# Kernel optimization log

Hardware: AMD Instinct MI355X
Metric: run time of the kernel (lower is better)

The kernel has to match this reference:

```python
import jax, jax.numpy as jnp
import numpy as np

N = 8192
E = 131072
IN = 512
H = 8
C = 128
HC = H * C
EPS = 1e-5
NEG_SLOPE = 0.2


def _gatv2(x, src, dst, Wl, bl, Wr, br, att, bias):
    """GATv2Conv (PyG semantics, concat=True, self-loops already in src/dst)."""
    n = x.shape[0]
    xl = (x @ Wl + bl).reshape(n, H, C)  # source transform (lin_l)
    xr = (x @ Wr + br).reshape(n, H, C)  # dest transform (lin_r)
    m = xl[src] + xr[dst]                # [E,H,C] per-edge message
    e = jnp.einsum('ehc,hc->eh', jax.nn.leaky_relu(m, NEG_SLOPE), att)  # [E,H]
    # segment softmax over destination nodes
    emax = jax.ops.segment_max(e, dst, num_segments=n)
    w = jnp.exp(e - emax[dst])
    denom = jax.ops.segment_sum(w, dst, num_segments=n)
    alpha = w / denom[dst]               # [E,H]
    out = jax.ops.segment_sum(alpha[:, :, None] * xl[src], dst, num_segments=n)
    return out.reshape(n, HC) + bias


def _bn(x, gamma, beta):
    mu = jnp.mean(x, axis=0)
    var = jnp.mean((x - mu) ** 2, axis=0)
    return (x - mu) * jax.lax.rsqrt(var + EPS) * gamma + beta


def setup_inputs() -> dict:
    key = jax.random.key(0)
    ks = jax.random.split(key, 16)
    s = 0.05
    return {
        'x': jax.random.normal(ks[0], (N, IN), jnp.float32),
        'edge_index': jax.random.randint(ks[1], (2, E), 0, N, jnp.int32),
        'W1l': jax.random.normal(ks[2], (IN, HC), jnp.float32) * s,
        'b1l': jnp.zeros((HC,), jnp.float32),
        'W1r': jax.random.normal(ks[3], (IN, HC), jnp.float32) * s,
        'b1r': jnp.zeros((HC,), jnp.float32),
        'att1': jax.random.normal(ks[4], (H, C), jnp.float32) * s,
        'bias1': jnp.zeros((HC,), jnp.float32),
        'g1': jnp.ones((HC,), jnp.float32),
        'beta1': jnp.zeros((HC,), jnp.float32),
        'W2l': jax.random.normal(ks[5], (HC, HC), jnp.float32) * s,
        'b2l': jnp.zeros((HC,), jnp.float32),
        'W2r': jax.random.normal(ks[6], (HC, HC), jnp.float32) * s,
        'b2r': jnp.zeros((HC,), jnp.float32),
        'att2': jax.random.normal(ks[7], (H, C), jnp.float32) * s,
        'bias2': jnp.zeros((HC,), jnp.float32),
        'g2': jnp.ones((HC,), jnp.float32),
        'beta2': jnp.zeros((HC,), jnp.float32),
    }


def reference(x, edge_index, W1l, b1l, W1r, b1r, att1, bias1, g1, beta1,
              W2l, b2l, W2r, b2r, att2, bias2, g2, beta2):
    n = x.shape[0]
    loops = jnp.arange(n, dtype=edge_index.dtype)
    src = jnp.concatenate([edge_index[0], loops])
    dst = jnp.concatenate([edge_index[1], loops])
    h = _gatv2(x, src, dst, W1l, b1l, W1r, b1r, att1, bias1)
    h = jax.nn.elu(_bn(h, g1, beta1))
    h = _gatv2(h, src, dst, W2l, b2l, W2r, b2r, att2, bias2)
    h = jax.nn.elu(_bn(h, g2, beta2))
    return h
```

## Files before the change

kernel.cpp:

```cpp
#include <hip/hip_runtime.h>
#include <stdint.h>

#define NN     8192
#define NEDGE  131072
#define NETOT  (NEDGE + NN)
#define K_IN   512
#define HC_    1024
#define NOUT   2048
#define BNEPS  1e-5f
#define SLOPE  0.2f

typedef __bf16 bf16x8 __attribute__((ext_vector_type(8)));
typedef float  f32x4  __attribute__((ext_vector_type(4)));
typedef float  f32x2  __attribute__((ext_vector_type(2)));

__device__ __forceinline__ float bf2f(unsigned short u) {
  union { uint32_t u; float f; } c; c.u = ((uint32_t)u) << 16; return c.f;
}
__device__ __forceinline__ unsigned short f2bf(float f) {
  union { float f; uint32_t u; } c; c.f = f;
  uint32_t r = c.u + 0x7fffu + ((c.u >> 16) & 1u);
  return (unsigned short)(r >> 16);
}
__device__ __forceinline__ f32x2 upk2(uint32_t u) {
  union { uint32_t u; float f; } a, b;
  a.u = u << 16; b.u = u & 0xffff0000u;
  f32x2 r; r.x = a.f; r.y = b.f; return r;
}

__device__ __forceinline__ void gload16(const void* g, void* l) {
  __builtin_amdgcn_global_load_lds(
      (const __attribute__((address_space(1))) uint32_t*)g,
      (__attribute__((address_space(3))) uint32_t*)l, 16, 0, 0);
}

#define SBAR() do { asm volatile("" ::: "memory"); __builtin_amdgcn_s_barrier(); asm volatile("" ::: "memory"); } while (0)

__global__ __launch_bounds__(256) void k_cvt_bf16(const float* __restrict__ in,
                                                  unsigned short* __restrict__ out, int n4) {
  int i = blockIdx.x * 256 + threadIdx.x;
  if (i >= n4) return;
  float4 v = *(const float4*)&in[(size_t)i * 4];
  ushort4 o;
  o.x = f2bf(v.x); o.y = f2bf(v.y); o.z = f2bf(v.z); o.w = f2bf(v.w);
  *(ushort4*)&out[(size_t)i * 4] = o;
}

__global__ __launch_bounds__(256) void k_transpose_bf16(const float* __restrict__ W,
                                                        unsigned short* __restrict__ Wt,
                                                        int K, int N) {
  __shared__ float tile[32][33];
  int n0 = blockIdx.x * 32, k0 = blockIdx.y * 32;
  int tx = threadIdx.x & 31, ty = threadIdx.x >> 5;
  for (int i = ty; i < 32; i += 8)
    tile[i][tx] = W[(size_t)(k0 + i) * N + n0 + tx];
  __syncthreads();
  for (int i = ty; i < 32; i += 8)
    Wt[(size_t)(n0 + i) * K + k0 + tx] = f2bf(tile[tx][i]);
}

__global__ __launch_bounds__(256) void k_hist(const int* __restrict__ ei, int* __restrict__ cnt) {
  int i = blockIdx.x * 256 + threadIdx.x;
  if (i >= NETOT) return;
  int d = (i < NEDGE) ? ei[NEDGE + i] : (i - NEDGE);
  atomicAdd(&cnt[d], 1);
}

__global__ __launch_bounds__(256) void k_scan(const int* __restrict__ cnt,
                                              int* __restrict__ rowptr,
                                              int* __restrict__ cursor) {
  __shared__ int part[256];
  int t = threadIdx.x;
  int base = t * 32;
  int s = 0;
  for (int i = 0; i < 32; ++i) s += cnt[base + i];
  part[t] = s;
  __syncthreads();
  for (int off = 1; off < 256; off <<= 1) {
    int u = (t >= off) ? part[t - off] : 0;
    __syncthreads();
    part[t] += u;
    __syncthreads();
  }
  int run = part[t] - s;
  for (int i = 0; i < 32; ++i) {
    rowptr[base + i] = run;
    cursor[base + i] = run;
    run += cnt[base + i];
  }
  if (t == 255) rowptr[NN] = run;
}

__global__ __launch_bounds__(256) void k_scatter(const int* __restrict__ ei,
                                                 int* __restrict__ cursor,
                                                 int* __restrict__ srcs) {
  int i = blockIdx.x * 256 + threadIdx.x;
  if (i >= NETOT) return;
  int s, d;
  if (i < NEDGE) { s = ei[i]; d = ei[NEDGE + i]; }
  else           { s = d = i - NEDGE; }
  int pos = atomicAdd(&cursor[d], 1);
  srcs[pos] = s;
}

__global__ __launch_bounds__(512, 2) void k_gemm256(const unsigned short* __restrict__ A,
                                                    const unsigned short* __restrict__ Bt,
                                                    const float* __restrict__ biasL,
                                                    const float* __restrict__ biasR,
                                                    unsigned short* __restrict__ C,
                                                    int K) {
  __shared__ unsigned short lA[2][256 * 64];
  __shared__ unsigned short lB[2][256 * 64];

  const int bid = blockIdx.x;
  const int xcd = bid & 7, idx = bid >> 3;
  const int m0 = (xcd * 4 + (idx & 3)) * 256;
  const int n0 = (idx >> 2) * 256;

  const int tid = threadIdx.x;
  const int l   = tid & 63;
  const int wv  = tid >> 6;
  const int wm  = wv >> 2, wn = wv & 3;
  const int l15 = l & 15, l4 = l >> 4;

  const int srow = tid >> 3;
  const int ssgk = (tid & 7) ^ (srow & 7);

  const f32x4 vzero = {0.f, 0.f, 0.f, 0.f};
  f32x4 acc[8][4];
#pragma unroll
  for (int i = 0; i < 8; ++i)
#pragma unroll
    for (int j = 0; j < 4; ++j) acc[i][j] = vzero;

  bf16x8 a2[8];
  bf16x8 bb[2][4];

  auto stageA = [&](int kt, int h) {
    const int buf = kt & 1;
    const size_t go = (size_t)(m0 + h * 128 + srow) * K + (size_t)kt * 64 + ssgk * 8;
    unsigned short* lp = &lA[buf][h * 8192 + tid * 8];
    gload16(&A[go], lp);
    gload16(&A[go + (size_t)64 * K], lp + 4096);
  };
  auto stageB = [&](int kt, int h) {
    const int buf = kt & 1;
    const size_t go = (size_t)(n0 + h * 128 + srow) * K + (size_t)kt * 64 + ssgk * 8;
    unsigned short* lp = &lB[buf][h * 8192 + tid * 8];
    gload16(&Bt[go], lp);
    gload16(&Bt[go + (size_t)64 * K], lp + 4096);
  };
  auto readA = [&](int buf, int qm) {
#pragma unroll
    for (int fm = 0; fm < 4; ++fm)
#pragma unroll
      for (int kk = 0; kk < 2; ++kk) {
        int r = wm * 128 + (qm * 4 + fm) * 16 + l15;
        int g = (kk * 4 + l4) ^ (r & 7);
        a2[fm * 2 + kk] = *(const bf16x8*)&lA[buf][r * 64 + g * 8];
      }
  };
  auto readB = [&](int buf, int qn) {
#pragma unroll
    for (int fn = 0; fn < 2; ++fn)
#pragma unroll
      for (int kk = 0; kk < 2; ++kk) {
        int r = wn * 64 + (qn * 2 + fn) * 16 + l15;
        int g = (kk * 4 + l4) ^ (r & 7);
        bb[qn][fn * 2 + kk] = *(const bf16x8*)&lB[buf][r * 64 + g * 8];
      }
  };
  auto quad = [&](int qm, int qn) {
    __builtin_amdgcn_s_setprio(1);
#pragma unroll
    for (int fm = 0; fm < 4; ++fm)
#pragma unroll
      for (int fn = 0; fn < 2; ++fn)
#pragma unroll
        for (int kk = 0; kk < 2; ++kk)
          acc[qm * 4 + fm][qn * 2 + fn] = __builtin_amdgcn_mfma_f32_16x16x32_bf16(
              a2[fm * 2 + kk], bb[qn][fn * 2 + kk], acc[qm * 4 + fm][qn * 2 + fn], 0, 0, 0);
    __builtin_amdgcn_s_setprio(0);
  };

  const int NT = K >> 6;

  stageA(0, 0); stageA(0, 1); stageB(0, 0); stageB(0, 1);
  if (NT > 1) stageA(1, 0);
  asm volatile("s_waitcnt vmcnt(2)" ::: "memory");
  SBAR();

  for (int t = 0; t < NT; ++t) {
    const int buf = t & 1;
    readA(buf, 0); readB(buf, 0);
    if (t + 1 < NT) stageA(t + 1, 1);
    SBAR();
    quad(0, 0);
    SBAR();
    readB(buf, 1);
    if (t + 1 < NT) stageB(t + 1, 0);
    SBAR();
    quad(0, 1);
    SBAR();
    readA(buf, 1);
    if (t + 1 < NT) stageB(t + 1, 1);
    SBAR();
    quad(1, 0);
    SBAR();
    if (t + 2 < NT) stageA(t + 2, 0);
    asm volatile("s_waitcnt vmcnt(2)" ::: "memory");
    SBAR();
    quad(1, 1);
    SBAR();
  }

  const float* bias = (n0 < HC_) ? biasL : (biasR - HC_);
#pragma unroll
  for (int fm = 0; fm < 8; ++fm) {
#pragma unroll
    for (int fn = 0; fn < 4; ++fn) {
      int col = n0 + wn * 64 + fn * 16 + l15;
      float bv = bias[col];
#pragma unroll
      for (int j = 0; j < 4; ++j) {
        int row = m0 + wm * 128 + fm * 16 + l4 * 4 + j;
        C[(size_t)row * NOUT + col] = f2bf(acc[fm][fn][j] + bv);
      }
    }
  }
}

__global__ __launch_bounds__(256) void k_edge_agg(const unsigned short* __restrict__ XLR,
                                                  const float* __restrict__ att,
                                                  const float* __restrict__ bias,
                                                  const int* __restrict__ rowptr,
                                                  const int* __restrict__ srcs,
                                                  float* __restrict__ out) {
  const int d   = blockIdx.x;
  const int tid = threadIdx.x;
  const int g   = tid >> 6;
  const int l   = tid & 63;
  const int c0  = l * 16;

  f32x2 attv[8], xrv[8];
  {
    const f32x2* ap = (const f32x2*)&att[c0];
#pragma unroll
    for (int q = 0; q < 8; ++q) attv[q] = ap[q];
    const uint4* rp = (const uint4*)&XLR[(size_t)d * NOUT + HC_ + c0];
    uint4 u0 = rp[0], u1 = rp[1];
    xrv[0] = upk2(u0.x); xrv[1] = upk2(u0.y); xrv[2] = upk2(u0.z); xrv[3] = upk2(u0.w);
    xrv[4] = upk2(u1.x); xrv[5] = upk2(u1.y); xrv[6] = upk2(u1.z); xrv[7] = upk2(u1.w);
  }

  f32x2 acc2[8];
#pragma unroll
  for (int j = 0; j < 8; ++j) acc2[j] = (f32x2){0.f, 0.f};
  float den = 0.f;

  const int beg = rowptr[d], end = rowptr[d + 1];
  int i = beg + g;
  uint4 u0n, u1n;
  if (i < end) {
    const uint4* rp = (const uint4*)&XLR[(size_t)srcs[i] * NOUT + c0];
    u0n = rp[0]; u1n = rp[1];
  }
  while (i < end) {
    uint4 u0 = u0n, u1 = u1n;
    int nx = i + 4;
    if (nx < end) {
      const uint4* rp = (const uint4*)&XLR[(size_t)srcs[nx] * NOUT + c0];
      u0n = rp[0]; u1n = rp[1];
    }
    f32x2 x[8];
    x[0] = upk2(u0.x); x[1] = upk2(u0.y); x[2] = upk2(u0.z); x[3] = upk2(u0.w);
    x[4] = upk2(u1.x); x[5] = upk2(u1.y); x[6] = upk2(u1.z); x[7] = upk2(u1.w);
    f32x2 ps = (f32x2){0.f, 0.f};
#pragma unroll
    for (int j = 0; j < 8; ++j) {
      f32x2 m  = x[j] + xrv[j];
      f32x2 lr = __builtin_elementwise_max(m, m * SLOPE);
      ps = lr * attv[j] + ps;
    }
    float p = ps.x + ps.y;
    p += __shfl_xor(p, 1);
    p += __shfl_xor(p, 2);
    p += __shfl_xor(p, 4);
    float wgt = __expf(p);
    den += wgt;
    f32x2 w2 = (f32x2){wgt, wgt};
#pragma unroll
    for (int j = 0; j < 8; ++j) acc2[j] = w2 * x[j] + acc2[j];
    i = nx;
  }

  __shared__ float sacc[4][64][17];
  __shared__ float sden[4][64];
#pragma unroll
  for (int j = 0; j < 8; ++j) {
    sacc[g][l][j * 2]     = acc2[j].x;
    sacc[g][l][j * 2 + 1] = acc2[j].y;
  }
  sden[g][l] = den;
  __syncthreads();

  const int c  = tid * 4;
  const int hl = (c >> 7) * 8;
  float dtot = sden[0][hl] + sden[1][hl] + sden[2][hl] + sden[3][hl];
  float inv  = 1.0f / dtot;
  float4 bv  = *(const float4*)&bias[c];
  float o[4];
#pragma unroll
  for (int j = 0; j < 4; ++j) {
    int cc = c + j, ll = cc >> 4, jj = cc & 15;
    float s = sacc[0][ll][jj] + sacc[1][ll][jj] + sacc[2][ll][jj] + sacc[3][ll][jj];
    o[j] = s * inv;
  }
  float4 ov = {o[0] + bv.x, o[1] + bv.y, o[2] + bv.z, o[3] + bv.w};
  *(float4*)&out[(size_t)d * HC_ + c] = ov;
}

__global__ __launch_bounds__(256) void k_colstats(const float* __restrict__ X,
                                                  float* __restrict__ stats) {
  int col = blockIdx.x * 256 + threadIdx.x;
  int r0 = blockIdx.y * 128;
  float s = 0.f, q = 0.f;
  for (int r = r0; r < r0 + 128; ++r) {
    float v = X[(size_t)r * HC_ + col];
    s += v;
    q += v * v;
  }
  atomicAdd(&stats[col], s);
  atomicAdd(&stats[HC_ + col], q);
}

template <bool OUT_BF16>
__global__ __launch_bounds__(256) void k_bn_elu(const float* __restrict__ X,
                                                const float* __restrict__ stats,
                                                const float* __restrict__ gamma,
                                                const float* __restrict__ beta,
                                                void* __restrict__ outp) {
  size_t idx = (size_t)blockIdx.x * 256 + threadIdx.x;
  size_t e0 = idx * 4;
  int col = (int)(e0 & (HC_ - 1));
  float4 xv = *(const float4*)&X[e0];
  float xs[4] = {xv.x, xv.y, xv.z, xv.w};
  float os[4];
  const float rn = 1.0f / (float)NN;
#pragma unroll
  for (int j = 0; j < 4; ++j) {
    int c = col + j;
    float mu = stats[c] * rn;
    float var = stats[HC_ + c] * rn - mu * mu;
    float v = (xs[j] - mu) * rsqrtf(var + BNEPS) * gamma[c] + beta[c];
    os[j] = v > 0.f ? v : (__expf(v) - 1.f);
  }
  if (OUT_BF16) {
    ushort4 o;
    o.x = f2bf(os[0]); o.y = f2bf(os[1]); o.z = f2bf(os[2]); o.w = f2bf(os[3]);
    *(ushort4*)&((unsigned short*)outp)[e0] = o;
  } else {
    float4 o = {os[0], os[1], os[2], os[3]};
    *(float4*)&((float*)outp)[e0] = o;
  }
}

extern "C" void kernel_launch(void* const* d_in, const int* in_sizes, int n_in,
                              void* d_out, int out_size, void* d_ws, size_t ws_size,
                              hipStream_t stream) {
  const float* x     = (const float*)d_in[0];
  const int*   ei    = (const int*)d_in[1];
  const float* W1l   = (const float*)d_in[2];
  const float* b1l   = (const float*)d_in[3];
  const float* W1r   = (const float*)d_in[4];
  const float* b1r   = (const float*)d_in[5];
  const float* att1  = (const float*)d_in[6];
  const float* bias1 = (const float*)d_in[7];
  const float* g1    = (const float*)d_in[8];
  const float* be1   = (const float*)d_in[9];
  const float* W2l   = (const float*)d_in[10];
  const float* b2l   = (const float*)d_in[11];
  const float* W2r   = (const float*)d_in[12];
  const float* b2r   = (const float*)d_in[13];
  const float* att2  = (const float*)d_in[14];
  const float* bias2 = (const float*)d_in[15];
  const float* g2    = (const float*)d_in[16];
  const float* be2   = (const float*)d_in[17];
  float* out = (float*)d_out;

  char* wsb = (char*)d_ws;
  size_t o = 0;
  auto alloc = [&](size_t b) {
    void* p = wsb + o;
    o = (o + b + 255) & ~(size_t)255;
    return p;
  };
  unsigned short* xbf  = (unsigned short*)alloc((size_t)NN * K_IN * 2);
  unsigned short* wT1  = (unsigned short*)alloc((size_t)NOUT * K_IN * 2);
  unsigned short* wT2  = (unsigned short*)alloc((size_t)NOUT * HC_ * 2);
  unsigned short* XLR  = (unsigned short*)alloc((size_t)NN * NOUT * 2);
  unsigned short* h1bf = (unsigned short*)alloc((size_t)NN * HC_ * 2);
  int* cnt     = (int*)alloc((size_t)NN * 4);
  int* rowptr  = (int*)alloc((size_t)(NN + 1) * 4);
  int* cursor  = (int*)alloc((size_t)NN * 4);
  int* srcs    = (int*)alloc((size_t)NETOT * 4);
  float* stats = (float*)alloc((size_t)2 * HC_ * 4);

  hipMemsetAsync(cnt, 0, (size_t)NN * 4, stream);
  hipMemsetAsync(stats, 0, (size_t)2 * HC_ * 4, stream);

  k_cvt_bf16<<<(NN * K_IN / 4 + 255) / 256, 256, 0, stream>>>(x, xbf, NN * K_IN / 4);
  k_transpose_bf16<<<dim3(HC_ / 32, K_IN / 32), 256, 0, stream>>>(W1l, wT1, K_IN, HC_);
  k_transpose_bf16<<<dim3(HC_ / 32, K_IN / 32), 256, 0, stream>>>(W1r, wT1 + (size_t)HC_ * K_IN, K_IN, HC_);
  k_transpose_bf16<<<dim3(HC_ / 32, HC_ / 32), 256, 0, stream>>>(W2l, wT2, HC_, HC_);
  k_transpose_bf16<<<dim3(HC_ / 32, HC_ / 32), 256, 0, stream>>>(W2r, wT2 + (size_t)HC_ * HC_, HC_, HC_);

  k_hist<<<(NETOT + 255) / 256, 256, 0, stream>>>(ei, cnt);
  k_scan<<<1, 256, 0, stream>>>(cnt, rowptr, cursor);
  k_scatter<<<(NETOT + 255) / 256, 256, 0, stream>>>(ei, cursor, srcs);

  k_gemm256<<<256, 512, 0, stream>>>(xbf, wT1, b1l, b1r, XLR, K_IN);
  k_edge_agg<<<NN, 256, 0, stream>>>(XLR, att1, bias1, rowptr, srcs, out);
  k_colstats<<<dim3(HC_ / 256, NN / 128), 256, 0, stream>>>(out, stats);
  k_bn_elu<true><<<NN * HC_ / 4 / 256, 256, 0, stream>>>(out, stats, g1, be1, h1bf);

  k_gemm256<<<256, 512, 0, stream>>>(h1bf, wT2, b2l, b2r, XLR, HC_);
  k_edge_agg<<<NN, 256, 0, stream>>>(XLR, att2, bias2, rowptr, srcs, out);
  hipMemsetAsync(stats, 0, (size_t)2 * HC_ * 4, stream);
  k_colstats<<<dim3(HC_ / 256, NN / 128), 256, 0, stream>>>(out, stats);
  k_bn_elu<false><<<NN * HC_ / 4 / 256, 256, 0, stream>>>(out, stats, g2, be2, out);
}
```

Before: 252.1 us.

## Assign one wavefront per destination node and store layer-1 activations in bf16

The edge aggregation kernel now gives each wavefront a whole destination node and processes four nodes per block. This removes the shared-memory cross-wave reduction and the block barrier, and it prefetches two source rows ahead. Layer-1 aggregation output is written as bf16 and reused in place for colstats and BN/ELU, which cuts the fp32 intermediate traffic. Weight transposes are merged into two launches via a z grid dimension. The trade-offs are less memory-level parallelism per node for high-degree nodes and extra bf16 rounding before batch-norm statistics.

```diff
diff --git a/kernel.cpp b/kernel.cpp
--- a/kernel.cpp
+++ b/kernel.cpp
@@ -12,7 +12,6 @@
 
 typedef __bf16 bf16x8 __attribute__((ext_vector_type(8)));
 typedef float  f32x4  __attribute__((ext_vector_type(4)));
-typedef float  f32x2  __attribute__((ext_vector_type(2)));
 
 __device__ __forceinline__ float bf2f(unsigned short u) {
   union { uint32_t u; float f; } c; c.u = ((uint32_t)u) << 16; return c.f;
@@ -22,10 +21,10 @@
   uint32_t r = c.u + 0x7fffu + ((c.u >> 16) & 1u);
   return (unsigned short)(r >> 16);
 }
-__device__ __forceinline__ f32x2 upk2(uint32_t u) {
+__device__ __forceinline__ void unpack2(uint32_t u, float& lo, float& hi) {
   union { uint32_t u; float f; } a, b;
   a.u = u << 16; b.u = u & 0xffff0000u;
-  f32x2 r; r.x = a.f; r.y = b.f; return r;
+  lo = a.f; hi = b.f;
 }
 
 __device__ __forceinline__ void gload16(const void* g, void* l) {
@@ -46,17 +45,20 @@
   *(ushort4*)&out[(size_t)i * 4] = o;
 }
 
-__global__ __launch_bounds__(256) void k_transpose_bf16(const float* __restrict__ W,
-                                                        unsigned short* __restrict__ Wt,
-                                                        int K, int N) {
+__global__ __launch_bounds__(256) void k_transpose2_bf16(const float* __restrict__ Wa,
+                                                         const float* __restrict__ Wb,
+                                                         unsigned short* __restrict__ Wt,
+                                                         int K, int N) {
   __shared__ float tile[32][33];
+  const float* W = blockIdx.z ? Wb : Wa;
+  unsigned short* dst = Wt + (size_t)blockIdx.z * N * K;
   int n0 = blockIdx.x * 32, k0 = blockIdx.y * 32;
   int tx = threadIdx.x & 31, ty = threadIdx.x >> 5;
   for (int i = ty; i < 32; i += 8)
     tile[i][tx] = W[(size_t)(k0 + i) * N + n0 + tx];
   __syncthreads();
   for (int i = ty; i < 32; i += 8)
-    Wt[(size_t)(n0 + i) * K + k0 + tx] = f2bf(tile[tx][i]);
+    dst[(size_t)(n0 + i) * K + k0 + tx] = f2bf(tile[tx][i]);
 }
 
 __global__ __launch_bounds__(256) void k_hist(const int* __restrict__ ei, int* __restrict__ cnt) {
@@ -230,103 +232,118 @@
   }
 }
 
+template <bool OUT_BF16>
 __global__ __launch_bounds__(256) void k_edge_agg(const unsigned short* __restrict__ XLR,
                                                   const float* __restrict__ att,
                                                   const float* __restrict__ bias,
                                                   const int* __restrict__ rowptr,
                                                   const int* __restrict__ srcs,
-                                                  float* __restrict__ out) {
-  const int d   = blockIdx.x;
+                                                  void* __restrict__ outp) {
   const int tid = threadIdx.x;
-  const int g   = tid >> 6;
+  const int d   = blockIdx.x * 4 + (tid >> 6);
   const int l   = tid & 63;
   const int c0  = l * 16;
 
-  f32x2 attv[8], xrv[8];
+  float attv[16], xrv[16];
   {
-    const f32x2* ap = (const f32x2*)&att[c0];
-#pragma unroll
-    for (int q = 0; q < 8; ++q) attv[q] = ap[q];
+    const float4* ap = (const float4*)&att[c0];
+#pragma unroll
+    for (int q = 0; q < 4; ++q) {
+      float4 v = ap[q];
+      attv[q * 4 + 0] = v.x; attv[q * 4 + 1] = v.y;
+      attv[q * 4 + 2] = v.z; attv[q * 4 + 3] = v.w;
+    }
     const uint4* rp = (const uint4*)&XLR[(size_t)d * NOUT + HC_ + c0];
     uint4 u0 = rp[0], u1 = rp[1];
-    xrv[0] = upk2(u0.x); xrv[1] = upk2(u0.y); xrv[2] = upk2(u0.z); xrv[3] = upk2(u0.w);
-    xrv[4] = upk2(u1.x); xrv[5] = upk2(u1.y); xrv[6] = upk2(u1.z); xrv[7] = upk2(u1.w);
-  }
-
-  f32x2 acc2[8];
-#pragma unroll
-  for (int j = 0; j < 8; ++j) acc2[j] = (f32x2){0.f, 0.f};
+    unpack2(u0.x, xrv[0], xrv[1]);   unpack2(u0.y, xrv[2], xrv[3]);
+    unpack2(u0.z, xrv[4], xrv[5]);   unpack2(u0.w, xrv[6], xrv[7]);
+    unpack2(u1.x, xrv[8], xrv[9]);   unpack2(u1.y, xrv[10], xrv[11]);
+    unpack2(u1.z, xrv[12], xrv[13]); unpack2(u1.w, xrv[14], xrv[15]);
+  }
+
+  float acc[16];
+#pragma unroll
+  for (int j = 0; j < 16; ++j) acc[j] = 0.f;
   float den = 0.f;
 
   const int beg = rowptr[d], end = rowptr[d + 1];
-  int i = beg + g;
-  uint4 u0n, u1n;
-  if (i < end) {
-    const uint4* rp = (const uint4*)&XLR[(size_t)srcs[i] * NOUT + c0];
-    u0n = rp[0]; u1n = rp[1];
-  }
-  while (i < end) {
-    uint4 u0 = u0n, u1 = u1n;
-    int nx = i + 4;
-    if (nx < end) {
-      const uint4* rp = (const uint4*)&XLR[(size_t)srcs[nx] * NOUT + c0];
-      u0n = rp[0]; u1n = rp[1];
-    }
-    f32x2 x[8];
-    x[0] = upk2(u0.x); x[1] = upk2(u0.y); x[2] = upk2(u0.z); x[3] = upk2(u0.w);
-    x[4] = upk2(u1.x); x[5] = upk2(u1.y); x[6] = upk2(u1.z); x[7] = upk2(u1.w);
-    f32x2 ps = (f32x2){0.f, 0.f};
-#pragma unroll
-    for (int j = 0; j < 8; ++j) {
-      f32x2 m  = x[j] + xrv[j];
-      f32x2 lr = __builtin_elementwise_max(m, m * SLOPE);
-      ps = lr * attv[j] + ps;
-    }
-    float p = ps.x + ps.y;
+  uint4 b0u0, b0u1, b1u0, b1u1;
+  {
+    const uint4* rp = (const uint4*)&XLR[(size_t)srcs[beg] * NOUT + c0];
+    b0u0 = rp[0]; b0u1 = rp[1];
+  }
+  if (beg + 1 < end) {
+    const uint4* rp = (const uint4*)&XLR[(size_t)srcs[beg + 1] * NOUT + c0];
+    b1u0 = rp[0]; b1u1 = rp[1];
+  }
+  int s2 = (beg + 2 < end) ? srcs[beg + 2] : 0;
+
+  for (int i = beg; i < end; ++i) {
+    uint4 u0 = b0u0, u1 = b0u1;
+    b0u0 = b1u0; b0u1 = b1u1;
+    if (i + 2 < end) {
+      const uint4* rp = (const uint4*)&XLR[(size_t)s2 * NOUT + c0];
+      b1u0 = rp[0]; b1u1 = rp[1];
+    }
+    s2 = (i + 3 < end) ? srcs[i + 3] : 0;
+
+    float x[16];
+    unpack2(u0.x, x[0], x[1]);   unpack2(u0.y, x[2], x[3]);
+    unpack2(u0.z, x[4], x[5]);   unpack2(u0.w, x[6], x[7]);
+    unpack2(u1.x, x[8], x[9]);   unpack2(u1.y, x[10], x[11]);
+    unpack2(u1.z, x[12], x[13]); unpack2(u1.w, x[14], x[15]);
+    float p = 0.f;
+#pragma unroll
+    for (int j = 0; j < 16; ++j) {
+      float m  = x[j] + xrv[j];
+      float lr = fmaxf(m, SLOPE * m);
+      p = fmaf(lr, attv[j], p);
+    }
     p += __shfl_xor(p, 1);
     p += __shfl_xor(p, 2);
     p += __shfl_xor(p, 4);
     float wgt = __expf(p);
     den += wgt;
-    f32x2 w2 = (f32x2){wgt, wgt};
-#pragma unroll
-    for (int j = 0; j < 8; ++j) acc2[j] = w2 * x[j] + acc2[j];
-    i = nx;
-  }
-
-  __shared__ float sacc[4][64][17];
-  __shared__ float sden[4][64];
-#pragma unroll
-  for (int j = 0; j < 8; ++j) {
-    sacc[g][l][j * 2]     = acc2[j].x;
-    sacc[g][l][j * 2 + 1] = acc2[j].y;
-  }
-  sden[g][l] = den;
-  __syncthreads();
-
-  const int c  = tid * 4;
-  const int hl = (c >> 7) * 8;
-  float dtot = sden[0][hl] + sden[1][hl] + sden[2][hl] + sden[3][hl];
-  float inv  = 1.0f / dtot;
-  float4 bv  = *(const float4*)&bias[c];
-  float o[4];
-#pragma unroll
-  for (int j = 0; j < 4; ++j) {
-    int cc = c + j, ll = cc >> 4, jj = cc & 15;
-    float s = sacc[0][ll][jj] + sacc[1][ll][jj] + sacc[2][ll][jj] + sacc[3][ll][jj];
-    o[j] = s * inv;
-  }
-  float4 ov = {o[0] + bv.x, o[1] + bv.y, o[2] + bv.z, o[3] + bv.w};
-  *(float4*)&out[(size_t)d * HC_ + c] = ov;
-}
-
-__global__ __launch_bounds__(256) void k_colstats(const float* __restrict__ X,
+#pragma unroll
+    for (int j = 0; j < 16; ++j) acc[j] = fmaf(wgt, x[j], acc[j]);
+  }
+
+  float inv = 1.0f / den;
+  if (OUT_BF16) {
+    unsigned short* op = (unsigned short*)outp + (size_t)d * HC_ + c0;
+#pragma unroll
+    for (int q = 0; q < 2; ++q) {
+      ushort4 o0, o1;
+      const float4 bv0 = ((const float4*)&bias[c0])[q * 2];
+      const float4 bv1 = ((const float4*)&bias[c0])[q * 2 + 1];
+      o0.x = f2bf(acc[q * 8 + 0] * inv + bv0.x); o0.y = f2bf(acc[q * 8 + 1] * inv + bv0.y);
+      o0.z = f2bf(acc[q * 8 + 2] * inv + bv0.z); o0.w = f2bf(acc[q * 8 + 3] * inv + bv0.w);
+      o1.x = f2bf(acc[q * 8 + 4] * inv + bv1.x); o1.y = f2bf(acc[q * 8 + 5] * inv + bv1.y);
+      o1.z = f2bf(acc[q * 8 + 6] * inv + bv1.z); o1.w = f2bf(acc[q * 8 + 7] * inv + bv1.w);
+      *(ushort4*)&op[q * 8]     = o0;
+      *(ushort4*)&op[q * 8 + 4] = o1;
+    }
+  } else {
+    float* op = (float*)outp + (size_t)d * HC_ + c0;
+#pragma unroll
+    for (int q = 0; q < 4; ++q) {
+      float4 bv = ((const float4*)&bias[c0])[q];
+      float4 o = {acc[q * 4 + 0] * inv + bv.x, acc[q * 4 + 1] * inv + bv.y,
+                  acc[q * 4 + 2] * inv + bv.z, acc[q * 4 + 3] * inv + bv.w};
+      *(float4*)&op[q * 4] = o;
+    }
+  }
+}
+
+template <bool IN_BF16>
+__global__ __launch_bounds__(256) void k_colstats(const void* __restrict__ Xp,
                                                   float* __restrict__ stats) {
   int col = blockIdx.x * 256 + threadIdx.x;
   int r0 = blockIdx.y * 128;
   float s = 0.f, q = 0.f;
   for (int r = r0; r < r0 + 128; ++r) {
-    float v = X[(size_t)r * HC_ + col];
+    float v = IN_BF16 ? bf2f(((const unsigned short*)Xp)[(size_t)r * HC_ + col])
+                      : ((const float*)Xp)[(size_t)r * HC_ + col];
     s += v;
     q += v * v;
   }
@@ -334,8 +351,8 @@
   atomicAdd(&stats[HC_ + col], q);
 }
 
-template <bool OUT_BF16>
-__global__ __launch_bounds__(256) void k_bn_elu(const float* __restrict__ X,
+template <bool IN_BF16, bool OUT_BF16>
+__global__ __launch_bounds__(256) void k_bn_elu(const void* __restrict__ Xp,
                                                 const float* __restrict__ stats,
                                                 const float* __restrict__ gamma,
                                                 const float* __restrict__ beta,
@@ -343,8 +360,14 @@
   size_t idx = (size_t)blockIdx.x * 256 + threadIdx.x;
   size_t e0 = idx * 4;
   int col = (int)(e0 & (HC_ - 1));
-  float4 xv = *(const float4*)&X[e0];
-  float xs[4] = {xv.x, xv.y, xv.z, xv.w};
+  float xs[4];
+  if (IN_BF16) {
+    ushort4 u = *(const ushort4*)&((const unsigned short*)Xp)[e0];
+    xs[0] = bf2f(u.x); xs[1] = bf2f(u.y); xs[2] = bf2f(u.z); xs[3] = bf2f(u.w);
+  } else {
+    float4 xv = *(const float4*)&((const float*)Xp)[e0];
+    xs[0] = xv.x; xs[1] = xv.y; xs[2] = xv.z; xs[3] = xv.w;
+  }
   float os[4];
   const float rn = 1.0f / (float)NN;
 #pragma unroll
@@ -399,7 +422,7 @@
   unsigned short* wT1  = (unsigned short*)alloc((size_t)NOUT * K_IN * 2);
   unsigned short* wT2  = (unsigned short*)alloc((size_t)NOUT * HC_ * 2);
   unsigned short* XLR  = (unsigned short*)alloc((size_t)NN * NOUT * 2);
-  unsigned short* h1bf = (unsigned short*)alloc((size_t)NN * HC_ * 2);
+  unsigned short* h0   = (unsigned short*)alloc((size_t)NN * HC_ * 2);
   int* cnt     = (int*)alloc((size_t)NN * 4);
   int* rowptr  = (int*)alloc((size_t)(NN + 1) * 4);
   int* cursor  = (int*)alloc((size_t)NN * 4);
@@ -410,23 +433,21 @@
   hipMemsetAsync(stats, 0, (size_t)2 * HC_ * 4, stream);
 
   k_cvt_bf16<<<(NN * K_IN / 4 + 255) / 256, 256, 0, stream>>>(x, xbf, NN * K_IN / 4);
-  k_transpose_bf16<<<dim3(HC_ / 32, K_IN / 32), 256, 0, stream>>>(W1l, wT1, K_IN, HC_);
-  k_transpose_bf16<<<dim3(HC_ / 32, K_IN / 32), 256, 0, stream>>>(W1r, wT1 + (size_t)HC_ * K_IN, K_IN, HC_);
-  k_transpose_bf16<<<dim3(HC_ / 32, HC_ / 32), 256, 0, stream>>>(W2l, wT2, HC_, HC_);
-  k_transpose_bf16<<<dim3(HC_ / 32, HC_ / 32), 256, 0, stream>>>(W2r, wT2 + (size_t)HC_ * HC_, HC_, HC_);
+  k_transpose2_bf16<<<dim3(HC_ / 32, K_IN / 32, 2), 256, 0, stream>>>(W1l, W1r, wT1, K_IN, HC_);
+  k_transpose2_bf16<<<dim3(HC_ / 32, HC_ / 32, 2), 256, 0, stream>>>(W2l, W2r, wT2, HC_, HC_);
 
   k_hist<<<(NETOT + 255) / 256, 256, 0, stream>>>(ei, cnt);
   k_scan<<<1, 256, 0, stream>>>(cnt, rowptr, cursor);
   k_scatter<<<(NETOT + 255) / 256, 256, 0, stream>>>(ei, cursor, srcs);
 
   k_gemm256<<<256, 512, 0, stream>>>(xbf, wT1, b1l, b1r, XLR, K_IN);
-  k_edge_agg<<<NN, 256, 0, stream>>>(XLR, att1, bias1, rowptr, srcs, out);
-  k_colstats<<<dim3(HC_ / 256, NN / 128), 256, 0, stream>>>(out, stats);
-  k_bn_elu<true><<<NN * HC_ / 4 / 256, 256, 0, stream>>>(out, stats, g1, be1, h1bf);
-
-  k_gemm256<<<256, 512, 0, stream>>>(h1bf, wT2, b2l, b2r, XLR, HC_);
-  k_edge_agg<<<NN, 256, 0, stream>>>(XLR, att2, bias2, rowptr, srcs, out);
+  k_edge_agg<true><<<NN / 4, 256, 0, stream>>>(XLR, att1, bias1, rowptr, srcs, h0);
+  k_colstats<true><<<dim3(HC_ / 256, NN / 128), 256, 0, stream>>>(h0, stats);
+  k_bn_elu<true, true><<<NN * HC_ / 4 / 256, 256, 0, stream>>>(h0, stats, g1, be1, h0);
+
+  k_gemm256<<<256, 512, 0, stream>>>(h0, wT2, b2l, b2r, XLR, HC_);
+  k_edge_agg<false><<<NN / 4, 256, 0, stream>>>(XLR, att2, bias2, rowptr, srcs, out);
   hipMemsetAsync(stats, 0, (size_t)2 * HC_ * 4, stream);
-  k_colstats<<<dim3(HC_ / 256, NN / 128), 256, 0, stream>>>(out, stats);
-  k_bn_elu<false><<<NN * HC_ / 4 / 256, 256, 0, stream>>>(out, stats, g2, be2, out);
-}
+  k_colstats<false><<<dim3(HC_ / 256, NN / 128), 256, 0, stream>>>(out, stats);
+  k_bn_elu<false, false><<<NN * HC_ / 4 / 256, 256, 0, stream>>>(out, stats, g2, be2, out);
+}
```

New measurement: 239.9 us. 4.8% less time.
